# Kernel optimization log

Measured on AMD Instinct MI355X. Metric: run time of the kernel, lower is better.

Reference implementation:

```python
import jax, jax.numpy as jnp
import numpy as np

NPATCH = 196
NWINDOW = 4
D_MODEL = 768
N_HEADS = 12
DIM_HEAD = 64
D_FF = 3072
B = 4
T = NPATCH * NWINDOW          # 784
M_RAW = 1024                  # raw memory length (> T, trimmed to T)
EPS = 1e-5


def make_mac_mask():
    # generate_mac_mask_matrix(NPATCH, NWINDOW, n_persistent=0, n_retrieved=NWINDOW)
    total = 2 * NWINDOW
    # frame-level mask: retrieved rows see everything; window row i sees
    # all retrieved frames + window frames 0..i (block-causal)
    r = np.arange(total)[:, None]
    c = np.arange(total)[None, :]
    fmask = (r < NWINDOW) | (c <= r)          # [total, total] bool
    mask = np.kron(fmask, np.ones((NPATCH, NPATCH), dtype=bool))
    return jnp.asarray(mask)                   # [2T, 2T] bool


def layernorm(x, g, b):
    mu = jnp.mean(x, axis=-1, keepdims=True)
    var = jnp.var(x, axis=-1, keepdims=True)
    return (x - mu) * jax.lax.rsqrt(var + EPS) * g + b


def setup_inputs() -> dict:
    key = jax.random.key(0)
    ks = jax.random.split(key, 10)
    s = lambda fan_in: 1.0 / np.sqrt(fan_in)
    inner = N_HEADS * DIM_HEAD
    return {
        "x": jax.random.normal(ks[0], (B, T, D_MODEL), jnp.float32),
        "memory": jax.random.normal(ks[1], (B, M_RAW, D_MODEL), jnp.float32),
        "ln_att_g": jnp.ones((D_MODEL,), jnp.float32),
        "ln_att_b": jnp.zeros((D_MODEL,), jnp.float32),
        "w_qkv": jax.random.normal(ks[2], (3 * inner, D_MODEL), jnp.float32) * s(D_MODEL),
        "w_out": jax.random.normal(ks[3], (D_MODEL, inner), jnp.float32) * s(inner),
        "b_out": jnp.zeros((D_MODEL,), jnp.float32),
        "ln1_g": jnp.ones((D_MODEL,), jnp.float32),
        "ln1_b": jnp.zeros((D_MODEL,), jnp.float32),
        "ln2_g": jnp.ones((D_MODEL,), jnp.float32),
        "ln2_b": jnp.zeros((D_MODEL,), jnp.float32),
        "w1": jax.random.normal(ks[4], (D_FF, D_MODEL), jnp.float32) * s(D_MODEL),
        "b1": jnp.zeros((D_FF,), jnp.float32),
        "w2": jax.random.normal(ks[5], (D_MODEL, D_FF), jnp.float32) * s(D_FF),
        "b2": jnp.zeros((D_MODEL,), jnp.float32),
        "mask": make_mac_mask(),
    }


def reference(x, memory, ln_att_g, ln_att_b, w_qkv, w_out, b_out,
              ln1_g, ln1_b, ln2_g, ln2_b, w1, b1, w2, b2, mask):
    Bsz, Tlen, D = x.shape
    mem = memory[:, :Tlen, :]                      # memory longer than T -> trim
    x_aug = jnp.concatenate([mem, x], axis=1)      # [B, 2T, D]
    x_aug = layernorm(x_aug, ln1_g, ln1_b)

    # --- Attention (has its own pre-LN inside the module) ---
    L = x_aug.shape[1]
    h = layernorm(x_aug, ln_att_g, ln_att_b)
    qkv = jnp.einsum("bld,ed->ble", h, w_qkv)      # [B, L, 3*inner]
    q, k, v = jnp.split(qkv, 3, axis=-1)
    def heads(t):
        return t.reshape(Bsz, L, N_HEADS, DIM_HEAD).transpose(0, 2, 1, 3)
    q, k, v = heads(q), heads(k), heads(v)          # [B, H, L, Dh]
    scale = DIM_HEAD ** -0.5
    dots = jnp.einsum("bhid,bhjd->bhij", q, k) * scale
    dots = jnp.where(mask[:L, :L], dots, -jnp.inf)
    attn = jax.nn.softmax(dots, axis=-1)
    out = jnp.einsum("bhij,bhjd->bhid", attn, v)
    out = out.transpose(0, 2, 1, 3).reshape(Bsz, L, N_HEADS * DIM_HEAD)
    att_out = jnp.einsum("ble,de->bld", out, w_out) + b_out

    x_aug = x_aug + att_out
    y2 = layernorm(x_aug, ln2_g, ln2_b)
    ff = jnp.einsum("bld,fd->blf", y2, w1) + b1
    ff = jax.nn.silu(ff)
    ff = jnp.einsum("blf,df->bld", ff, w2) + b2
    x_aug = x_aug + ff
    return x_aug[:, Tlen:, :]                       # [B, T, D]
```

## Files before the change

kernel.cpp:

```cpp
#include <hip/hip_runtime.h>
#include <cstdint>

typedef __bf16 bf16;
typedef __bf16 bf16x4 __attribute__((ext_vector_type(4)));
typedef __bf16 bf16x8 __attribute__((ext_vector_type(8)));
typedef float f32x4 __attribute__((ext_vector_type(4)));

#define AS1 __attribute__((address_space(1)))
#define AS3 __attribute__((address_space(3)))

__device__ __forceinline__ void load16_lds(const void* gp, void* lds_base_wave_uniform) {
    __builtin_amdgcn_global_load_lds((AS1 void*)((void*)gp),
                                     (AS3 void*)lds_base_wave_uniform, 16, 0, 0);
}

__global__ __launch_bounds__(256) void prep_ln_split(
    const float* __restrict__ x, const float* __restrict__ memory,
    const float* __restrict__ g1, const float* __restrict__ b1,
    const float* __restrict__ ga, const float* __restrict__ ba,
    float* __restrict__ xres, bf16* __restrict__ hH,
    const float* __restrict__ wp0, bf16* __restrict__ wh0, bf16* __restrict__ wl0,
    const float* __restrict__ wp1, bf16* __restrict__ wh1, bf16* __restrict__ wl1,
    const float* __restrict__ wp2, bf16* __restrict__ wh2, bf16* __restrict__ wl2,
    const float* __restrict__ wp3, bf16* __restrict__ wh3, bf16* __restrict__ wl3)
{
    const int t = threadIdx.x;
    if (blockIdx.x >= 6272) {
        const int n0q = 442368, n1q = 147456, n2q = 589824;
        const int total = 1769472;
        const int stride = 2048 * 256;
        for (int i = (blockIdx.x - 6272) * 256 + t; i < total; i += stride) {
            const float* sp; bf16 *hp, *lp; int j = i;
            if (j < n0q) { sp = wp0; hp = wh0; lp = wl0; }
            else if ((j -= n0q) < n1q) { sp = wp1; hp = wh1; lp = wl1; }
            else if ((j -= n1q) < n2q) { sp = wp2; hp = wh2; lp = wl2; }
            else { j -= n2q; sp = wp3; hp = wh3; lp = wl3; }
            float4 v4 = reinterpret_cast<const float4*>(sp)[j];
            bf16x4 hi, lo;
            hi[0] = (bf16)v4.x; lo[0] = (bf16)(v4.x - (float)hi[0]);
            hi[1] = (bf16)v4.y; lo[1] = (bf16)(v4.y - (float)hi[1]);
            hi[2] = (bf16)v4.z; lo[2] = (bf16)(v4.z - (float)hi[2]);
            hi[3] = (bf16)v4.w; lo[3] = (bf16)(v4.w - (float)hi[3]);
            reinterpret_cast<bf16x4*>(hp)[j] = hi;
            reinterpret_cast<bf16x4*>(lp)[j] = lo;
        }
        return;
    }

    const int row = blockIdx.x;
    const int b = row / 1568, l = row - b * 1568;
    const float* src = (l < 784) ? (memory + ((size_t)b * 1024 + l) * 768)
                                 : (x + ((size_t)b * 784 + (l - 784)) * 768);
    const int lane = t & 63, wv = t >> 6;
    __shared__ float red[8];

    float v[3];
#pragma unroll
    for (int i = 0; i < 3; ++i) v[i] = src[i * 256 + t];

    float s = v[0] + v[1] + v[2];
    float s2 = v[0] * v[0] + v[1] * v[1] + v[2] * v[2];
#pragma unroll
    for (int off = 1; off < 64; off <<= 1) { s += __shfl_xor(s, off, 64); s2 += __shfl_xor(s2, off, 64); }
    if (lane == 0) { red[wv] = s; red[4 + wv] = s2; }
    __syncthreads();
    s = red[0] + red[1] + red[2] + red[3];
    s2 = red[4] + red[5] + red[6] + red[7];
    float mu = s * (1.0f / 768.0f);
    float var = s2 * (1.0f / 768.0f) - mu * mu;
    float rs = rsqrtf(fmaxf(var, 0.0f) + 1e-5f);

    float w[3];
#pragma unroll
    for (int i = 0; i < 3; ++i) {
        int c = i * 256 + t;
        w[i] = (v[i] - mu) * rs * g1[c] + b1[c];
    }
    if (l >= 784) {
        float* xr = xres + ((size_t)b * 784 + (l - 784)) * 768;
#pragma unroll
        for (int i = 0; i < 3; ++i) xr[i * 256 + t] = w[i];
    }

    s = w[0] + w[1] + w[2];
    s2 = w[0] * w[0] + w[1] * w[1] + w[2] * w[2];
#pragma unroll
    for (int off = 1; off < 64; off <<= 1) { s += __shfl_xor(s, off, 64); s2 += __shfl_xor(s2, off, 64); }
    __syncthreads();
    if (lane == 0) { red[wv] = s; red[4 + wv] = s2; }
    __syncthreads();
    s = red[0] + red[1] + red[2] + red[3];
    s2 = red[4] + red[5] + red[6] + red[7];
    float mu2 = s * (1.0f / 768.0f);
    float var2 = s2 * (1.0f / 768.0f) - mu2 * mu2;
    float rs2 = rsqrtf(fmaxf(var2, 0.0f) + 1e-5f);

    bf16* hh_ = hH + (size_t)row * 768;
#pragma unroll
    for (int i = 0; i < 3; ++i) {
        int c = i * 256 + t;
        float hv = (w[i] - mu2) * rs2 * ga[c] + ba[c];
        hh_[c] = (bf16)hv;
    }
}

__global__ __launch_bounds__(256, 2) void gemm_qkv(
    const bf16* __restrict__ Ah,
    const bf16* __restrict__ Bh, const bf16* __restrict__ Bl,
    int M, int N, int K,
    bf16* __restrict__ Ch, bf16* __restrict__ Cl)
{
    __shared__ __align__(16) bf16 Ahs[2 * 256 * 32];
    __shared__ __align__(16) bf16 Bhs[2 * 128 * 32], Bls[2 * 128 * 32];
    const int t = threadIdx.x, lane = t & 63, wv = t >> 6;

    const int nx = gridDim.x, ny = gridDim.y;
    int orig = blockIdx.x + nx * blockIdx.y;
    int nwg = nx * ny;
    int q = nwg >> 3, rr8 = nwg & 7;
    int xcd = orig & 7, pos = orig >> 3;
    int wgid = (xcd < rr8 ? xcd * (q + 1) : rr8 * (q + 1) + (xcd - rr8) * q) + pos;
    int bx = wgid % nx, by = wgid / nx;

    const int row0 = by * 256, col0 = bx * 128;
    const int ro = (wv >> 1) * 128, co = (wv & 1) * 64;
    const int l15 = lane & 15, q8 = lane >> 4;
    const int cs = (q8 ^ (l15 & 3)) * 8;

    f32x4 acc[8][4] = {};

    for (int k0 = 0; k0 < K; k0 += 64) {
#pragma unroll
        for (int h = 0; h < 2; ++h) {
            const int kk = k0 + h * 32;
#pragma unroll
            for (int it = 0; it < 4; ++it) {
                int f = it * 256 + t;
                int r = f >> 2;
                int kc = ((f & 3) ^ (r & 3)) * 8;
                int ra = row0 + r; if (ra >= M) ra = M - 1;
                size_t oa = (size_t)ra * K + kk + kc;
                size_t lb = (size_t)(h * 1024 + it * 256 + wv * 64) * 8;
                load16_lds(Ah + oa, Ahs + lb);
            }
#pragma unroll
            for (int it = 0; it < 2; ++it) {
                int f = it * 256 + t;
                int r = f >> 2;
                int kc = ((f & 3) ^ (r & 3)) * 8;
                size_t ob = (size_t)(col0 + r) * K + kk + kc;
                size_t lb = (size_t)(h * 512 + it * 256 + wv * 64) * 8;
                load16_lds(Bh + ob, Bhs + lb);
                load16_lds(Bl + ob, Bls + lb);
            }
        }
        asm volatile("s_waitcnt vmcnt(0)" ::: "memory");
        __syncthreads();

#pragma unroll
        for (int h = 0; h < 2; ++h) {
            const int ab = h * 8192, bb = h * 4096;
            bf16x8 bh[4], bl[4];
#pragma unroll
            for (int j = 0; j < 4; ++j) {
                int o = bb + (co + j * 16 + l15) * 32 + cs;
                bh[j] = *(const bf16x8*)&Bhs[o];
                bl[j] = *(const bf16x8*)&Bls[o];
            }
#pragma unroll
            for (int i = 0; i < 8; ++i) {
                int o = ab + (ro + i * 16 + l15) * 32 + cs;
                bf16x8 ah = *(const bf16x8*)&Ahs[o];
#pragma unroll
                for (int j = 0; j < 4; ++j) {
                    acc[i][j] = __builtin_amdgcn_mfma_f32_16x16x32_bf16(ah, bl[j], acc[i][j], 0, 0, 0);
                    acc[i][j] = __builtin_amdgcn_mfma_f32_16x16x32_bf16(ah, bh[j], acc[i][j], 0, 0, 0);
                }
            }
        }
        __syncthreads();
    }

#pragma unroll
    for (int i = 0; i < 8; ++i)
#pragma unroll
        for (int j = 0; j < 4; ++j)
#pragma unroll
            for (int r = 0; r < 4; ++r) {
                int row = row0 + ro + i * 16 + q8 * 4 + r;
                int col = col0 + co + j * 16 + l15;
                if (row >= M) continue;
                float v = acc[i][j][r];
                size_t idx = (size_t)row * N + col;
                bf16 hh = (bf16)v;
                Ch[idx] = hh;
                if (col < 768) Cl[idx] = (bf16)(v - (float)hh);
            }
}

template <int MODE, int ORD>
__global__ __launch_bounds__(256, 2) void gemm_pl(
    const bf16* __restrict__ Ah,
    const bf16* __restrict__ Bh, const bf16* __restrict__ Bl,
    int M, int N, int K,
    const float* __restrict__ bias,
    float* __restrict__ Cf, bf16* __restrict__ Ch)
{
    __shared__ __align__(16) bf16 Ahs[2 * 128 * 32];
    __shared__ __align__(16) bf16 Bhs[2 * 128 * 32], Bls[2 * 128 * 32];
    const int t = threadIdx.x, lane = t & 63, wv = t >> 6;

    const int nx = gridDim.x, ny = gridDim.y;
    int orig = blockIdx.x + nx * blockIdx.y;
    int nwg = nx * ny;
    int q = nwg >> 3, rr8 = nwg & 7;
    int xcd = orig & 7, pos = orig >> 3;
    int wgid = (xcd < rr8 ? xcd * (q + 1) : rr8 * (q + 1) + (xcd - rr8) * q) + pos;
    int bx, by;
    if (ORD == 0) { bx = wgid % nx; by = wgid / nx; }
    else          { by = wgid % ny; bx = wgid / ny; }

    const int row0 = by * 128, col0 = bx * 128;
    const int ro = (wv >> 1) * 64, co = (wv & 1) * 64;
    const int Kc = K / gridDim.z;
    const int kbeg = blockIdx.z * Kc, kend = kbeg + Kc;
    const int l15 = lane & 15, q8 = lane >> 4;
    const int cs = (q8 ^ (l15 & 3)) * 8;

    f32x4 acc[4][4] = {};

    for (int k0 = kbeg; k0 < kend; k0 += 64) {
#pragma unroll
        for (int h = 0; h < 2; ++h) {
            const int kk = k0 + h * 32;
#pragma unroll
            for (int it = 0; it < 2; ++it) {
                int f = it * 256 + t;
                int r = f >> 2;
                int kc = ((f & 3) ^ (r & 3)) * 8;
                int ra = row0 + r; if (ra >= M) ra = M - 1;
                size_t oa = (size_t)ra * K + kk + kc;
                size_t ob = (size_t)(col0 + r) * K + kk + kc;
                size_t lb = (size_t)(h * 512 + it * 256 + wv * 64) * 8;
                load16_lds(Ah + oa, Ahs + lb);
                load16_lds(Bh + ob, Bhs + lb);
                load16_lds(Bl + ob, Bls + lb);
            }
        }
        asm volatile("s_waitcnt vmcnt(0)" ::: "memory");
        __syncthreads();
#pragma unroll
        for (int h = 0; h < 2; ++h) {
            const int hb = h * 4096;
            bf16x8 ah[4], bh[4], bl[4];
#pragma unroll
            for (int i = 0; i < 4; ++i) {
                int o = hb + (ro + i * 16 + l15) * 32 + cs;
                ah[i] = *(const bf16x8*)&Ahs[o];
            }
#pragma unroll
            for (int j = 0; j < 4; ++j) {
                int o = hb + (co + j * 16 + l15) * 32 + cs;
                bh[j] = *(const bf16x8*)&Bhs[o];
                bl[j] = *(const bf16x8*)&Bls[o];
            }
#pragma unroll
            for (int i = 0; i < 4; ++i)
#pragma unroll
                for (int j = 0; j < 4; ++j) {
                    acc[i][j] = __builtin_amdgcn_mfma_f32_16x16x32_bf16(ah[i], bl[j], acc[i][j], 0, 0, 0);
                    acc[i][j] = __builtin_amdgcn_mfma_f32_16x16x32_bf16(ah[i], bh[j], acc[i][j], 0, 0, 0);
                }
        }
        __syncthreads();
    }

    const size_t zoff = (size_t)blockIdx.z * M * N;
#pragma unroll
    for (int i = 0; i < 4; ++i)
#pragma unroll
        for (int j = 0; j < 4; ++j)
#pragma unroll
            for (int r = 0; r < 4; ++r) {
                int row = row0 + ro + i * 16 + (lane >> 4) * 4 + r;
                int col = col0 + co + j * 16 + (lane & 15);
                if (row >= M) continue;
                float v = acc[i][j][r];
                size_t idx = (size_t)row * N + col;
                if (MODE == 1) {
                    Cf[zoff + idx] = v;
                } else if (MODE == 2) {
                    v += bias[col];
                    v = v / (1.0f + __expf(-v));
                    Ch[idx] = (bf16)v;
                } else {
                    unsafeAtomicAdd(&Cf[idx], v);
                }
            }
}

__global__ __launch_bounds__(256, 3) void attn_kernel(
    const bf16* __restrict__ qh_, const bf16* __restrict__ ql_,
    bf16* __restrict__ oh_)
{
    const int hh = blockIdx.x % 12, b = blockIdx.x / 12;
    const int w = blockIdx.y >> 2, g = blockIdx.y & 3;
    const int kmax = (5 + w) * 196, nkt = (kmax + 31) / 32;
    const int t = threadIdx.x, lane = t & 63, wv = t >> 6;
    const int tile = g * 4 + wv;
    const int l15 = lane & 15, q8 = lane >> 4;

    __shared__ __align__(16) bf16 Ks_h[2][32 * 64];
    __shared__ __align__(16) bf16 Vt_h[2][64 * 40];
    __shared__ __align__(16) bf16 Pl_h[4][16 * 40];

    const size_t bbase = (size_t)b * 1568 * 2304;

    const int srow = t >> 3;
    const int sc8 = (t & 7) * 8;
    const int scsrc = sc8 ^ ((srow & 7) * 8);

    int tcl = tile > 12 ? 12 : tile;
    int qr0 = tcl * 16 + l15; if (qr0 > 195) qr0 = 195;
    const size_t qoff = bbase + (size_t)(784 + w * 196 + qr0) * 2304 + hh * 64 + q8 * 8;
    bf16x8 qfh[2], qfl[2];
#pragma unroll
    for (int p = 0; p < 2; ++p) {
        qfh[p] = *(const bf16x8*)(qh_ + qoff + p * 32);
        qfl[p] = *(const bf16x8*)(ql_ + qoff + p * 32);
    }

    float l_i[4] = {0.f, 0.f, 0.f, 0.f};
    f32x4 oacc[4];
#pragma unroll
    for (int nd = 0; nd < 4; ++nd) oacc[nd] = f32x4{0.f, 0.f, 0.f, 0.f};

    auto stage_issue = [&](int kt2, int bufn, bf16x8& vreg) {
        const size_t kb = bbase + (size_t)(kt2 * 32 + srow) * 2304 + 768 + (size_t)hh * 64;
        load16_lds(qh_ + kb + scsrc, &Ks_h[bufn][wv * 512]);
        vreg = *(const bf16x8*)(qh_ + kb + 768 + sc8);
    };
    auto write_V = [&](int bufn, const bf16x8& vreg) {
#pragma unroll
        for (int j = 0; j < 8; ++j) {
            int d = sc8 + j;
            int keyx = srow ^ (((d >> 3) & 3) * 8);
            Vt_h[bufn][d * 40 + keyx] = vreg[j];
        }
    };

    {
        bf16x8 v0;
        stage_issue(0, 0, v0);
        write_V(0, v0);
        asm volatile("s_waitcnt vmcnt(0)" ::: "memory");
        __syncthreads();
    }

    const float CEXP = 0.18033688011112042f;

    for (int kt = 0; kt < nkt; ++kt) {
        const int cur = kt & 1, nxt = cur ^ 1;
        int kt2 = kt + 1; if (kt2 >= nkt) kt2 = nkt - 1;
        bf16x8 vnext;
        stage_issue(kt2, nxt, vnext);

        if (tile <= 12) {
            bf16x8 kfh[2][2], vth[4];
#pragma unroll
            for (int nb = 0; nb < 2; ++nb)
#pragma unroll
                for (int p = 0; p < 2; ++p) {
                    int row = nb * 16 + l15;
                    int c = (p * 32 + q8 * 8) ^ ((row & 7) * 8);
                    kfh[nb][p] = *(const bf16x8*)&Ks_h[cur][row * 64 + c];
                }
#pragma unroll
            for (int nd = 0; nd < 4; ++nd) {
                int d = nd * 16 + l15;
                int k8 = (q8 * 8) ^ (((d >> 3) & 3) * 8);
                vth[nd] = *(const bf16x8*)&Vt_h[cur][d * 40 + k8];
            }

            f32x4 s0a = {0.f,0.f,0.f,0.f}, s0b = {0.f,0.f,0.f,0.f};
            f32x4 s1a = {0.f,0.f,0.f,0.f}, s1b = {0.f,0.f,0.f,0.f};
            __builtin_amdgcn_s_setprio(1);
            s0a = __builtin_amdgcn_mfma_f32_16x16x32_bf16(qfl[0], kfh[0][0], s0a, 0, 0, 0);
            s1a = __builtin_amdgcn_mfma_f32_16x16x32_bf16(qfl[0], kfh[1][0], s1a, 0, 0, 0);
            s0b = __builtin_amdgcn_mfma_f32_16x16x32_bf16(qfl[1], kfh[0][1], s0b, 0, 0, 0);
            s1b = __builtin_amdgcn_mfma_f32_16x16x32_bf16(qfl[1], kfh[1][1], s1b, 0, 0, 0);
            s0a = __builtin_amdgcn_mfma_f32_16x16x32_bf16(qfh[0], kfh[0][0], s0a, 0, 0, 0);
            s1a = __builtin_amdgcn_mfma_f32_16x16x32_bf16(qfh[0], kfh[1][0], s1a, 0, 0, 0);
            s0b = __builtin_amdgcn_mfma_f32_16x16x32_bf16(qfh[1], kfh[0][1], s0b, 0, 0, 0);
            s1b = __builtin_amdgcn_mfma_f32_16x16x32_bf16(qfh[1], kfh[1][1], s1b, 0, 0, 0);
            __builtin_amdgcn_s_setprio(0);
            f32x4 s0 = s0a + s0b, s1 = s1a + s1b;

            const int key0 = kt * 32 + l15;
            const bool m0 = (key0 >= kmax), m1 = (key0 + 16 >= kmax);
#pragma unroll
            for (int r = 0; r < 4; ++r) {
                float p0 = m0 ? 0.0f : exp2f(s0[r] * CEXP);
                float p1 = m1 ? 0.0f : exp2f(s1[r] * CEXP);
                l_i[r] += p0 + p1;
                int pr = q8 * 4 + r;
                Pl_h[wv][pr * 40 + l15] = (bf16)p0;
                Pl_h[wv][pr * 40 + 16 + l15] = (bf16)p1;
            }
            asm volatile("s_waitcnt lgkmcnt(0)" ::: "memory");
            bf16x8 pfh = *(const bf16x8*)&Pl_h[wv][l15 * 40 + q8 * 8];
            __builtin_amdgcn_s_setprio(1);
#pragma unroll
            for (int nd = 0; nd < 4; ++nd)
                oacc[nd] = __builtin_amdgcn_mfma_f32_16x16x32_bf16(pfh, vth[nd], oacc[nd], 0, 0, 0);
            __builtin_amdgcn_s_setprio(0);
        }

        write_V(nxt, vnext);
        asm volatile("s_waitcnt vmcnt(0)" ::: "memory");
        __syncthreads();
    }

    if (tile <= 12) {
#pragma unroll
        for (int r = 0; r < 4; ++r) {
            float s = l_i[r];
#pragma unroll
            for (int off = 1; off < 16; off <<= 1) s += __shfl_xor(s, off, 64);
            int qr = tile * 16 + q8 * 4 + r;
            if (qr >= 196) continue;
            float inv = 1.0f / s;
            size_t row = (size_t)b * 784 + w * 196 + qr;
#pragma unroll
            for (int nd = 0; nd < 4; ++nd) {
                float ov = oacc[nd][r] * inv;
                size_t idx = row * 768 + hh * 64 + nd * 16 + l15;
                oh_[idx] = (bf16)ov;
            }
        }
    }
}

__global__ __launch_bounds__(256) void ln2_resid(
    const float* __restrict__ xres, const float* __restrict__ attP,
    const float* __restrict__ bo,
    const float* __restrict__ g2, const float* __restrict__ b2,
    const float* __restrict__ b2ff,
    float* __restrict__ y, bf16* __restrict__ y2H,
    float* __restrict__ dout)
{
    const int row = blockIdx.x;
    const size_t MN = (size_t)3136 * 768;
    const float* xr = xres + (size_t)row * 768;
    const float* a0 = attP + (size_t)row * 768;
    const float* a1 = attP + MN + (size_t)row * 768;
    const int t = threadIdx.x, lane = t & 63, wv = t >> 6;
    __shared__ float red[8];

    float v[3];
    float* yr = y + (size_t)row * 768;
    float* dr = dout + (size_t)row * 768;
#pragma unroll
    for (int i = 0; i < 3; ++i) {
        int c = i * 256 + t;
        v[i] = xr[c] + a0[c] + a1[c] + bo[c];
        yr[c] = v[i];
        dr[c] = v[i] + b2ff[c];
    }
    float s = v[0] + v[1] + v[2];
    float s2 = v[0] * v[0] + v[1] * v[1] + v[2] * v[2];
#pragma unroll
    for (int off = 1; off < 64; off <<= 1) { s += __shfl_xor(s, off, 64); s2 += __shfl_xor(s2, off, 64); }
    if (lane == 0) { red[wv] = s; red[4 + wv] = s2; }
    __syncthreads();
    s = red[0] + red[1] + red[2] + red[3];
    s2 = red[4] + red[5] + red[6] + red[7];
    float mu = s * (1.0f / 768.0f);
    float var = s2 * (1.0f / 768.0f) - mu * mu;
    float rs = rsqrtf(fmaxf(var, 0.0f) + 1e-5f);

    bf16* yh = y2H + (size_t)row * 768;
#pragma unroll
    for (int i = 0; i < 3; ++i) {
        int c = i * 256 + t;
        float yv = (v[i] - mu) * rs * g2[c] + b2[c];
        yh[c] = (bf16)yv;
    }
}

extern "C" void kernel_launch(void* const* d_in, const int* in_sizes, int n_in,
                              void* d_out, int out_size, void* d_ws, size_t ws_size,
                              hipStream_t stream)
{
    (void)in_sizes; (void)n_in; (void)out_size; (void)ws_size;
    const float* x        = (const float*)d_in[0];
    const float* memory   = (const float*)d_in[1];
    const float* ln_att_g = (const float*)d_in[2];
    const float* ln_att_b = (const float*)d_in[3];
    const float* w_qkv    = (const float*)d_in[4];
    const float* w_out    = (const float*)d_in[5];
    const float* b_out    = (const float*)d_in[6];
    const float* ln1_g    = (const float*)d_in[7];
    const float* ln1_b    = (const float*)d_in[8];
    const float* ln2_g    = (const float*)d_in[9];
    const float* ln2_b    = (const float*)d_in[10];
    const float* w1       = (const float*)d_in[11];
    const float* b1       = (const float*)d_in[12];
    const float* w2       = (const float*)d_in[13];
    const float* b2       = (const float*)d_in[14];

    char* ws = (char*)d_ws;
    const size_t SZF  = (size_t)3136 * 768 * 4;
    const size_t SZP  = (size_t)3136 * 768 * 2;
    const size_t SZHP = (size_t)6272 * 768 * 2;
    const size_t SZQP = (size_t)6272 * 2304 * 2;
    const size_t SZFP = (size_t)3136 * 3072 * 2;

    float* xres = (float*)(ws);
    bf16* hH  = (bf16*)(ws + SZF);
    bf16* aoH = (bf16*)(ws + SZF);
    bf16* y2H = (bf16*)(ws + SZF);
    const size_t OQ = SZF + 2 * SZHP;
    bf16* qkvH = (bf16*)(ws + OQ);
    bf16* qkvL = (bf16*)(ws + OQ + SZQP);
    float* y    = (float*)(ws + OQ);
    float* attP = (float*)(ws + OQ + SZF);
    bf16* ffH  = (bf16*)(ws + OQ + SZF);
    const size_t OW = OQ + 2 * SZQP;
    bf16* wqH = (bf16*)(ws + OW);
    bf16* wqL = (bf16*)(ws + OW + 3538944);
    bf16* woH = (bf16*)(ws + OW + 2 * 3538944);
    bf16* woL = (bf16*)(ws + OW + 2 * 3538944 + 1179648);
    bf16* w1H = (bf16*)(ws + OW + 2 * 3538944 + 2 * 1179648);
    bf16* w1L = (bf16*)(ws + OW + 2 * 3538944 + 2 * 1179648 + 4718592);
    bf16* w2H = (bf16*)(ws + OW + 2 * 3538944 + 2 * 1179648 + 2 * 4718592);
    bf16* w2L = (bf16*)(ws + OW + 2 * 3538944 + 2 * 1179648 + 3 * 4718592);

    prep_ln_split<<<8320, 256, 0, stream>>>(x, memory, ln1_g, ln1_b, ln_att_g, ln_att_b,
                                            xres, hH,
                                            w_qkv, wqH, wqL, w_out, woH, woL,
                                            w1, w1H, w1L, w2, w2H, w2L);

    gemm_qkv<<<dim3(18, 25), 256, 0, stream>>>(hH, wqH, wqL, 6272, 2304, 768,
                                               qkvH, qkvL);

    attn_kernel<<<dim3(48, 16), 256, 0, stream>>>(qkvH, qkvL, aoH);

    gemm_pl<1, 0><<<dim3(6, 25, 2), 256, 0, stream>>>(aoH, woH, woL, 3136, 768, 768,
                                                      nullptr, attP, nullptr);

    ln2_resid<<<3136, 256, 0, stream>>>(xres, attP, b_out, ln2_g, ln2_b, b2,
                                        y, y2H, (float*)d_out);

    gemm_pl<2, 1><<<dim3(24, 25), 256, 0, stream>>>(y2H, w1H, w1L, 3136, 3072, 768,
                                                    b1, nullptr, ffH);

    gemm_pl<3, 0><<<dim3(6, 25, 4), 256, 0, stream>>>(ffH, w2H, w2L, 3136, 768, 3072,
                                                      nullptr, (float*)d_out, nullptr);
}
```

Before: 365.3 us.

## Replace QKV GEMM with generic 128-tile kernel and deepen split-K

The dedicated 256x128-tile QKV GEMM is removed and replaced by the generic 128x128 gemm_pl template with a new MODE 0 epilogue that writes the hi/lo bf16 split. The out-projection split-K goes from 2 to 4 partial buffers, with ln2_resid summing four partials, and the FFN down-projection split-K goes from 4 to 8 atomic slices. The aim is more workgroups to fill the GPU's compute units. The cost is smaller tiles with less data reuse, extra partial-buffer traffic, and more atomic adds.

```diff
diff --git a/kernel.cpp b/kernel.cpp
--- a/kernel.cpp
+++ b/kernel.cpp
@@ -104,107 +104,13 @@
     }
 }
 
-__global__ __launch_bounds__(256, 2) void gemm_qkv(
-    const bf16* __restrict__ Ah,
-    const bf16* __restrict__ Bh, const bf16* __restrict__ Bl,
-    int M, int N, int K,
-    bf16* __restrict__ Ch, bf16* __restrict__ Cl)
-{
-    __shared__ __align__(16) bf16 Ahs[2 * 256 * 32];
-    __shared__ __align__(16) bf16 Bhs[2 * 128 * 32], Bls[2 * 128 * 32];
-    const int t = threadIdx.x, lane = t & 63, wv = t >> 6;
-
-    const int nx = gridDim.x, ny = gridDim.y;
-    int orig = blockIdx.x + nx * blockIdx.y;
-    int nwg = nx * ny;
-    int q = nwg >> 3, rr8 = nwg & 7;
-    int xcd = orig & 7, pos = orig >> 3;
-    int wgid = (xcd < rr8 ? xcd * (q + 1) : rr8 * (q + 1) + (xcd - rr8) * q) + pos;
-    int bx = wgid % nx, by = wgid / nx;
-
-    const int row0 = by * 256, col0 = bx * 128;
-    const int ro = (wv >> 1) * 128, co = (wv & 1) * 64;
-    const int l15 = lane & 15, q8 = lane >> 4;
-    const int cs = (q8 ^ (l15 & 3)) * 8;
-
-    f32x4 acc[8][4] = {};
-
-    for (int k0 = 0; k0 < K; k0 += 64) {
-#pragma unroll
-        for (int h = 0; h < 2; ++h) {
-            const int kk = k0 + h * 32;
-#pragma unroll
-            for (int it = 0; it < 4; ++it) {
-                int f = it * 256 + t;
-                int r = f >> 2;
-                int kc = ((f & 3) ^ (r & 3)) * 8;
-                int ra = row0 + r; if (ra >= M) ra = M - 1;
-                size_t oa = (size_t)ra * K + kk + kc;
-                size_t lb = (size_t)(h * 1024 + it * 256 + wv * 64) * 8;
-                load16_lds(Ah + oa, Ahs + lb);
-            }
-#pragma unroll
-            for (int it = 0; it < 2; ++it) {
-                int f = it * 256 + t;
-                int r = f >> 2;
-                int kc = ((f & 3) ^ (r & 3)) * 8;
-                size_t ob = (size_t)(col0 + r) * K + kk + kc;
-                size_t lb = (size_t)(h * 512 + it * 256 + wv * 64) * 8;
-                load16_lds(Bh + ob, Bhs + lb);
-                load16_lds(Bl + ob, Bls + lb);
-            }
-        }
-        asm volatile("s_waitcnt vmcnt(0)" ::: "memory");
-        __syncthreads();
-
-#pragma unroll
-        for (int h = 0; h < 2; ++h) {
-            const int ab = h * 8192, bb = h * 4096;
-            bf16x8 bh[4], bl[4];
-#pragma unroll
-            for (int j = 0; j < 4; ++j) {
-                int o = bb + (co + j * 16 + l15) * 32 + cs;
-                bh[j] = *(const bf16x8*)&Bhs[o];
-                bl[j] = *(const bf16x8*)&Bls[o];
-            }
-#pragma unroll
-            for (int i = 0; i < 8; ++i) {
-                int o = ab + (ro + i * 16 + l15) * 32 + cs;
-                bf16x8 ah = *(const bf16x8*)&Ahs[o];
-#pragma unroll
-                for (int j = 0; j < 4; ++j) {
-                    acc[i][j] = __builtin_amdgcn_mfma_f32_16x16x32_bf16(ah, bl[j], acc[i][j], 0, 0, 0);
-                    acc[i][j] = __builtin_amdgcn_mfma_f32_16x16x32_bf16(ah, bh[j], acc[i][j], 0, 0, 0);
-                }
-            }
-        }
-        __syncthreads();
-    }
-
-#pragma unroll
-    for (int i = 0; i < 8; ++i)
-#pragma unroll
-        for (int j = 0; j < 4; ++j)
-#pragma unroll
-            for (int r = 0; r < 4; ++r) {
-                int row = row0 + ro + i * 16 + q8 * 4 + r;
-                int col = col0 + co + j * 16 + l15;
-                if (row >= M) continue;
-                float v = acc[i][j][r];
-                size_t idx = (size_t)row * N + col;
-                bf16 hh = (bf16)v;
-                Ch[idx] = hh;
-                if (col < 768) Cl[idx] = (bf16)(v - (float)hh);
-            }
-}
-
 template <int MODE, int ORD>
 __global__ __launch_bounds__(256, 2) void gemm_pl(
     const bf16* __restrict__ Ah,
     const bf16* __restrict__ Bh, const bf16* __restrict__ Bl,
     int M, int N, int K,
     const float* __restrict__ bias,
-    float* __restrict__ Cf, bf16* __restrict__ Ch)
+    float* __restrict__ Cf, bf16* __restrict__ Ch, bf16* __restrict__ Cl)
 {
     __shared__ __align__(16) bf16 Ahs[2 * 128 * 32];
     __shared__ __align__(16) bf16 Bhs[2 * 128 * 32], Bls[2 * 128 * 32];
@@ -287,7 +193,11 @@
                 if (row >= M) continue;
                 float v = acc[i][j][r];
                 size_t idx = (size_t)row * N + col;
-                if (MODE == 1) {
+                if (MODE == 0) {
+                    bf16 hh = (bf16)v;
+                    Ch[idx] = hh;
+                    if (col < 768) Cl[idx] = (bf16)(v - (float)hh);
+                } else if (MODE == 1) {
                     Cf[zoff + idx] = v;
                 } else if (MODE == 2) {
                     v += bias[col];
@@ -454,6 +364,8 @@
     const float* xr = xres + (size_t)row * 768;
     const float* a0 = attP + (size_t)row * 768;
     const float* a1 = attP + MN + (size_t)row * 768;
+    const float* a2 = attP + 2 * MN + (size_t)row * 768;
+    const float* a3 = attP + 3 * MN + (size_t)row * 768;
     const int t = threadIdx.x, lane = t & 63, wv = t >> 6;
     __shared__ float red[8];
 
@@ -463,7 +375,7 @@
 #pragma unroll
     for (int i = 0; i < 3; ++i) {
         int c = i * 256 + t;
-        v[i] = xr[c] + a0[c] + a1[c] + bo[c];
+        v[i] = xr[c] + (a0[c] + a1[c]) + (a2[c] + a3[c]) + bo[c];
         yr[c] = v[i];
         dr[c] = v[i] + b2ff[c];
     }
@@ -511,10 +423,8 @@
 
     char* ws = (char*)d_ws;
     const size_t SZF  = (size_t)3136 * 768 * 4;
-    const size_t SZP  = (size_t)3136 * 768 * 2;
     const size_t SZHP = (size_t)6272 * 768 * 2;
     const size_t SZQP = (size_t)6272 * 2304 * 2;
-    const size_t SZFP = (size_t)3136 * 3072 * 2;
 
     float* xres = (float*)(ws);
     bf16* hH  = (bf16*)(ws + SZF);
@@ -541,20 +451,20 @@
                                             w_qkv, wqH, wqL, w_out, woH, woL,
                                             w1, w1H, w1L, w2, w2H, w2L);
 
-    gemm_qkv<<<dim3(18, 25), 256, 0, stream>>>(hH, wqH, wqL, 6272, 2304, 768,
-                                               qkvH, qkvL);
+    gemm_pl<0, 0><<<dim3(18, 49), 256, 0, stream>>>(hH, wqH, wqL, 6272, 2304, 768,
+                                                    nullptr, nullptr, qkvH, qkvL);
 
     attn_kernel<<<dim3(48, 16), 256, 0, stream>>>(qkvH, qkvL, aoH);
 
-    gemm_pl<1, 0><<<dim3(6, 25, 2), 256, 0, stream>>>(aoH, woH, woL, 3136, 768, 768,
-                                                      nullptr, attP, nullptr);
+    gemm_pl<1, 0><<<dim3(6, 25, 4), 256, 0, stream>>>(aoH, woH, woL, 3136, 768, 768,
+                                                      nullptr, attP, nullptr, nullptr);
 
     ln2_resid<<<3136, 256, 0, stream>>>(xres, attP, b_out, ln2_g, ln2_b, b2,
                                         y, y2H, (float*)d_out);
 
     gemm_pl<2, 1><<<dim3(24, 25), 256, 0, stream>>>(y2H, w1H, w1L, 3136, 3072, 768,
-                                                    b1, nullptr, ffH);
-
-    gemm_pl<3, 0><<<dim3(6, 25, 4), 256, 0, stream>>>(ffH, w2H, w2L, 3136, 768, 3072,
-                                                      nullptr, (float*)d_out, nullptr);
-}
+                                                    b1, nullptr, ffH, nullptr);
+
+    gemm_pl<3, 0><<<dim3(6, 25, 8), 256, 0, stream>>>(ffH, w2H, w2L, 3136, 768, 3072,
+                                                      nullptr, (float*)d_out, nullptr, nullptr);
+}
```

Result: slower. 394.5 us (+8.0%).
